# Performance work log

Hardware: AMD Instinct MI355X
Metric: run time of the kernel (lower is better)

## Reference

```python
import jax, jax.numpy as jnp
import numpy as np

N = 100000   # nodes
E = 1600000  # directed edges (avg degree 16)
H = 64       # MODEL_HIDDEN_CHANNELS


def setup_inputs() -> dict:
    key = jax.random.key(0)
    ks = jax.random.split(key, 6)
    x = jax.random.normal(ks[0], (N, 1), dtype=jnp.float32)
    edge_index = jax.random.randint(ks[1], (2, E), 0, N, dtype=jnp.int32)
    w1 = jax.random.normal(ks[2], (1, H), dtype=jnp.float32) * 0.5
    b1 = jnp.zeros((H,), dtype=jnp.float32)
    w2 = jax.random.normal(ks[3], (H, H), dtype=jnp.float32) * (1.0 / np.sqrt(H))
    b2 = jnp.zeros((H,), dtype=jnp.float32)
    wfc = jax.random.normal(ks[4], (H, 1), dtype=jnp.float32) * (1.0 / np.sqrt(H))
    bfc = jnp.zeros((1,), dtype=jnp.float32)
    return {"x": x, "edge_index": edge_index, "w1": w1, "b1": b1,
            "w2": w2, "b2": b2, "wfc": wfc, "bfc": bfc}


def _gcn_conv(x, src, dst, norm, W, b, n):
    # PyG GCNConv: h = x @ W, then scatter-add of norm-weighted messages at dst, + bias
    h = x @ W                                   # [n, out]
    msg = h[src] * norm[:, None]                # gather + scale, [e, out]
    agg = jax.ops.segment_sum(msg, dst, num_segments=n)
    return agg + b


def reference(x, edge_index, w1, b1, w2, b2, wfc, bfc):
    n = x.shape[0]
    # add self-loops (PyG GCNConv default)
    loops = jnp.arange(n, dtype=edge_index.dtype)
    src = jnp.concatenate([edge_index[0], loops])
    dst = jnp.concatenate([edge_index[1], loops])
    # symmetric degree normalization D^{-1/2} A_hat D^{-1/2}
    deg = jax.ops.segment_sum(jnp.ones(src.shape[0], dtype=x.dtype), dst, num_segments=n)
    dinv = jnp.where(deg > 0, jax.lax.rsqrt(deg), 0.0)
    norm = dinv[src] * dinv[dst]
    h = jax.nn.relu(_gcn_conv(x, src, dst, norm, w1, b1, n))
    h = jax.nn.relu(_gcn_conv(h, src, dst, norm, w2, b2, n))
    out = h @ wfc + bfc                         # [n, 1]
    return out.reshape(-1)
```

## Files before the change

kernel.cpp:

```cpp
#include <hip/hip_runtime.h>


#define HCH 64
#define CHUNK 8192
#define BSH 7
#define BSZ 128
#define NBMAX 1024

__device__ __forceinline__ void lds_addf(float* p, float v) {
    __hip_atomic_fetch_add(p, v, __ATOMIC_RELAXED, __HIP_MEMORY_SCOPE_WORKGROUP);
}

__global__ __launch_bounds__(512) void k_init(int nb, int cap,
                                              int* __restrict__ cursor,
                                              int* __restrict__ ov_cursor,
                                              const float* __restrict__ w1,
                                              const float* __restrict__ b1,
                                              const float* __restrict__ w2,
                                              float* __restrict__ P) {
    __shared__ float part[8][4][HCH];
    __shared__ float fsum;
    int t = threadIdx.x;
    for (int i = t; i < nb; i += 512) cursor[i] = i * cap;
    if (t == 0) { *ov_cursor = 0; fsum = 0.f; }
    int j = t & 63, seg = t >> 6;
    float pp = 0.f, pm = 0.f, bp = 0.f, bm = 0.f;
#pragma unroll
    for (int kk = 0; kk < 8; kk++) {
        int k = seg * 8 + kk;
        float w = w1[k], b = b1[k], v = w2[k * HCH + j];
        if (w > 0.f) { pp += w * v; bp += b * v; }
        else if (w < 0.f) { pm += w * v; bm += b * v; }
        else { float rb = b > 0.f ? b : 0.f; bp += rb * v; bm += rb * v; }
    }
    part[seg][0][j] = pp; part[seg][1][j] = pm;
    part[seg][2][j] = bp; part[seg][3][j] = bm;
    __syncthreads();
    if (t < 4 * HCH) {
        int c = t >> 6, jj = t & 63;
        float s = 0.f;
#pragma unroll
        for (int g = 0; g < 8; g++) s += part[g][c][jj];
        P[t] = s;
        if (c >= 2) lds_addf(&fsum, fabsf(s));
    }
    __syncthreads();
    if (t == 0) P[4 * HCH] = fsum;
}

__global__ __launch_bounds__(512) void k_place(const int* __restrict__ src,
                                               const int* __restrict__ dst, int e,
                                               int nb, int cap,
                                               int* __restrict__ cursor,
                                               int* __restrict__ ov_cursor,
                                               int* __restrict__ packed,
                                               int2* __restrict__ ovbuf) {
    __shared__ int h[NBMAX];
    __shared__ int scanE[NBMAX];
    __shared__ int basel[NBMAX];
    __shared__ int avail[NBMAX];
    __shared__ int slpv[CHUNK];
    __shared__ short ssb[CHUNK];
    __shared__ int wsum[8];
    int t = threadIdx.x;
    for (int i = t; i < NBMAX; i += 512) h[i] = 0;
    __syncthreads();
    int cbase = blockIdx.x * CHUNK;
    int rem = min(e - cbase, CHUNK);

#pragma unroll
    for (int k = 0; k < CHUNK / 2048; k++) {
        int li = (k * 512 + t) * 4;
        if (li + 3 < rem) {
            int4 d4 = *(const int4*)(dst + cbase + li);
            atomicAdd(&h[d4.x >> BSH], 1);
            atomicAdd(&h[d4.y >> BSH], 1);
            atomicAdd(&h[d4.z >> BSH], 1);
            atomicAdd(&h[d4.w >> BSH], 1);
        } else {
            for (int q = li; q < rem && q < li + 4; q++)
                atomicAdd(&h[dst[cbase + q] >> BSH], 1);
        }
    }
    __syncthreads();

    int v0 = h[2 * t], v1 = h[2 * t + 1];
    for (int i = t; i < nb; i += 512) {
        int my = h[i];
        int av = 0, base = 0;
        if (my) {
            base = atomicAdd(&cursor[i], my);
            int room = (i + 1) * cap - base;
            av = room < 0 ? 0 : (room > my ? my : room);
        }
        basel[i] = base;
        avail[i] = av;
    }
    int lane = t & 63, wid = t >> 6;
    int s = v0 + v1;
    int incl = s;
#pragma unroll
    for (int d = 1; d < 64; d <<= 1) {
        int o = __shfl_up(incl, d, 64);
        if (lane >= d) incl += o;
    }
    if (lane == 63) wsum[wid] = incl;
    __syncthreads();
    if (t < 8) {
        int v = wsum[t];
        int inc2 = v;
#pragma unroll
        for (int d = 1; d < 8; d <<= 1) {
            int o = __shfl_up(inc2, d, 8);
            if (t >= d) inc2 += o;
        }
        wsum[t] = inc2 - v;
    }
    for (int i = t; i < NBMAX; i += 512) h[i] = 0;
    __syncthreads();
    int excl = incl - s + wsum[wid];
    scanE[2 * t] = excl;
    scanE[2 * t + 1] = excl + v0;
    __syncthreads();

#pragma unroll
    for (int k = 0; k < CHUNK / 2048; k++) {
        int li = (k * 512 + t) * 4;
        if (li + 3 < rem) {
            int4 s4 = *(const int4*)(src + cbase + li);
            int4 d4 = *(const int4*)(dst + cbase + li);
#pragma unroll
            for (int q = 0; q < 4; q++) {
                int sv = (q == 0) ? s4.x : (q == 1) ? s4.y : (q == 2) ? s4.z : s4.w;
                int dv = (q == 0) ? d4.x : (q == 1) ? d4.y : (q == 2) ? d4.z : d4.w;
                int b = dv >> BSH;
                int pos = scanE[b] + atomicAdd(&h[b], 1);
                slpv[pos] = sv | ((dv & (BSZ - 1)) << 17);
                ssb[pos] = (short)b;
            }
        } else {
            for (int q = li; q < rem && q < li + 4; q++) {
                int sv = src[cbase + q], dv = dst[cbase + q];
                int b = dv >> BSH;
                int pos = scanE[b] + atomicAdd(&h[b], 1);
                slpv[pos] = sv | ((dv & (BSZ - 1)) << 17);
                ssb[pos] = (short)b;
            }
        }
    }
    __syncthreads();

    for (int jj = t; jj < rem; jj += 512) {
        int b = ssb[jj];
        int loc = jj - scanE[b];
        int pv = slpv[jj];
        if (loc < avail[b]) {
            packed[basel[b] + loc] = pv;
        } else {
            int op = atomicAdd(ov_cursor, 1);
            ovbuf[op] = make_int2(pv & 0x1FFFF, (b << BSH) | (pv >> 17));
        }
    }
}

__global__ __launch_bounds__(512) void k_bdeg(const int* __restrict__ packed,
                                              const int* __restrict__ cursor,
                                              const int* __restrict__ ov_cursor,
                                              const int2* __restrict__ ovbuf,
                                              int cap, const float* __restrict__ x, int n,
                                              float* __restrict__ dinv,
                                              float* __restrict__ y) {
    __shared__ int cnt[BSZ];
    int bk = blockIdx.x, t = threadIdx.x;
    int bbase = bk * cap;
    int bcnt = min(cursor[bk] - bbase, cap);
    if (t < BSZ) cnt[t] = 0;
    __syncthreads();
    for (int base = 0; base < bcnt; base += 2048) {
        int i0 = base + t * 4;
        if (i0 + 3 < bcnt) {
            int4 p = *(const int4*)(packed + bbase + i0);
            atomicAdd(&cnt[p.x >> 17], 1);
            atomicAdd(&cnt[p.y >> 17], 1);
            atomicAdd(&cnt[p.z >> 17], 1);
            atomicAdd(&cnt[p.w >> 17], 1);
        } else {
            for (int i = i0; i < bcnt && i < i0 + 4; i++)
                atomicAdd(&cnt[packed[bbase + i] >> 17], 1);
        }
    }
    int ovc = *ov_cursor;
    for (int i = t; i < ovc; i += 512) {
        int2 o = ovbuf[i];
        if ((o.y >> BSH) == bk) atomicAdd(&cnt[o.y & (BSZ - 1)], 1);
    }
    __syncthreads();
    int node = (bk << BSH) + t;
    if (t < BSZ && node < n) {
        float dv = rsqrtf((float)(cnt[t] + 1));
        dinv[node] = dv;
        y[node] = dv * x[node];
    }
}

__global__ __launch_bounds__(512) void k_bagg1(const int* __restrict__ packed,
                                               const int* __restrict__ cursor,
                                               const int* __restrict__ ov_cursor,
                                               const int2* __restrict__ ovbuf,
                                               int cap,
                                               const float* __restrict__ dinv,
                                               const float* __restrict__ y, int n,
                                               float2* __restrict__ val2) {
    __shared__ float acc[BSZ];
    int bk = blockIdx.x, t = threadIdx.x;
    int bbase = bk * cap;
    int bcnt = min(cursor[bk] - bbase, cap);
    if (t < BSZ) acc[t] = 0.f;
    __syncthreads();
    for (int base = 0; base < bcnt; base += 2048) {
        int i0 = base + t * 4;
        if (i0 + 3 < bcnt) {
            int4 p = *(const int4*)(packed + bbase + i0);
            float y0 = y[p.x & 0x1FFFF], y1 = y[p.y & 0x1FFFF];
            float y2 = y[p.z & 0x1FFFF], y3 = y[p.w & 0x1FFFF];
            lds_addf(&acc[p.x >> 17], y0);
            lds_addf(&acc[p.y >> 17], y1);
            lds_addf(&acc[p.z >> 17], y2);
            lds_addf(&acc[p.w >> 17], y3);
        } else {
            for (int i = i0; i < bcnt && i < i0 + 4; i++) {
                int p = packed[bbase + i];
                lds_addf(&acc[p >> 17], y[p & 0x1FFFF]);
            }
        }
    }
    int ovc = *ov_cursor;
    for (int i = t; i < ovc; i += 512) {
        int2 o = ovbuf[i];
        if ((o.y >> BSH) == bk) lds_addf(&acc[o.y & (BSZ - 1)], y[o.x]);
    }
    __syncthreads();
    int node = (bk << BSH) + t;
    if (t < BSZ && node < n) {
        float dv = dinv[node];
        float s = dv * (acc[t] + y[node]);
        val2[node] = make_float2(dv * s, dv);
    }
}

__global__ __launch_bounds__(512) void k_bagg2(const int* __restrict__ packed,
                                               const int* __restrict__ cursor,
                                               const int* __restrict__ ov_cursor,
                                               const int2* __restrict__ ovbuf,
                                               int cap, const float2* __restrict__ val2,
                                               const float* __restrict__ dinv,
                                               const float* __restrict__ P,
                                               const float* __restrict__ b2,
                                               const float* __restrict__ wfc,
                                               const float* __restrict__ bfc,
                                               float* __restrict__ out, int n) {
    __shared__ float aa[2 * BSZ];
    __shared__ float cc[2 * BSZ];
    __shared__ float sP[4 * HCH], sb2[HCH], swfc[HCH];
    __shared__ float sflag;
    int bk = blockIdx.x, t = threadIdx.x;
    int bbase = bk * cap;
    int bcnt = min(cursor[bk] - bbase, cap);
    if (t < 2 * BSZ) { aa[t] = 0.f; cc[t] = 0.f; }
    if (t < 4 * HCH) sP[t] = P[t];
    if (t >= 256 && t < 320) sb2[t - 256] = b2[t - 256];
    if (t >= 320 && t < 384) swfc[t - 320] = wfc[t - 320];
    if (t == 448) sflag = P[4 * HCH];
    __syncthreads();
    bool useB = sflag != 0.f;
    for (int base = 0; base < bcnt; base += 2048) {
        int i0 = base + t * 4;
        if (i0 + 3 < bcnt) {
            int4 p = *(const int4*)(packed + bbase + i0);
            float2 v0 = val2[p.x & 0x1FFFF], v1 = val2[p.y & 0x1FFFF];
            float2 v2 = val2[p.z & 0x1FFFF], v3 = val2[p.w & 0x1FFFF];
            int o0 = (v0.x > 0.f ? 0 : BSZ) + (p.x >> 17);
            int o1 = (v1.x > 0.f ? 0 : BSZ) + (p.y >> 17);
            int o2 = (v2.x > 0.f ? 0 : BSZ) + (p.z >> 17);
            int o3 = (v3.x > 0.f ? 0 : BSZ) + (p.w >> 17);
            lds_addf(&aa[o0], v0.x); lds_addf(&aa[o1], v1.x);
            lds_addf(&aa[o2], v2.x); lds_addf(&aa[o3], v3.x);
            if (useB) {
                lds_addf(&cc[o0], v0.y); lds_addf(&cc[o1], v1.y);
                lds_addf(&cc[o2], v2.y); lds_addf(&cc[o3], v3.y);
            }
        } else {
            for (int i = i0; i < bcnt && i < i0 + 4; i++) {
                int p = packed[bbase + i];
                float2 v = val2[p & 0x1FFFF];
                int off = (v.x > 0.f ? 0 : BSZ) + (p >> 17);
                lds_addf(&aa[off], v.x);
                if (useB) lds_addf(&cc[off], v.y);
            }
        }
    }
    int ovc = *ov_cursor;
    for (int i = t; i < ovc; i += 512) {
        int2 o = ovbuf[i];
        if ((o.y >> BSH) == bk) {
            float2 v = val2[o.x];
            int off = (v.x > 0.f ? 0 : BSZ) + (o.y & (BSZ - 1));
            lds_addf(&aa[off], v.x);
            if (useB) lds_addf(&cc[off], v.y);
        }
    }
    __syncthreads();
    int node = (bk << BSH) + t;
    if (t >= BSZ || node >= n) return;
    float a_p = aa[t], a_m = aa[BSZ + t], c_p = cc[t], c_m = cc[BSZ + t];
    float2 sv = val2[node];
    if (sv.x > 0.f) { a_p += sv.x; c_p += sv.y; }
    else            { a_m += sv.x; c_m += sv.y; }
    float dv = dinv[node];
    float acc = 0.f;
#pragma unroll 8
    for (int j = 0; j < HCH; j++) {
        float z = dv * (a_p * sP[j] + a_m * sP[HCH + j] +
                        c_p * sP[2 * HCH + j] + c_m * sP[3 * HCH + j]) + sb2[j];
        z = z > 0.f ? z : 0.f;
        acc += z * swfc[j];
    }
    out[node] = acc + bfc[0];
}

extern "C" void kernel_launch(void* const* d_in, const int* in_sizes, int n_in,
                              void* d_out, int out_size, void* d_ws, size_t ws_size,
                              hipStream_t stream) {
    const float* x   = (const float*)d_in[0];
    const int*   ei  = (const int*)d_in[1];
    const float* w1  = (const float*)d_in[2];
    const float* b1  = (const float*)d_in[3];
    const float* w2  = (const float*)d_in[4];
    const float* b2  = (const float*)d_in[5];
    const float* wfc = (const float*)d_in[6];
    const float* bfc = (const float*)d_in[7];
    float* out = (float*)d_out;

    const int n = in_sizes[0];
    const int e = in_sizes[1] / 2;
    const int* src = ei;
    const int* dst = ei + e;

    const int nb = (n + BSZ - 1) >> BSH;
    int avg = (e + nb - 1) / nb;
    int cap = ((avg + avg / 4 + 64) + 15) & ~15;

    auto al = [](size_t v) { return (v + 255) & ~(size_t)255; };
    char* ws = (char*)d_ws;
    size_t o = 0;
    int* cursor    = (int*)(ws + o);  o = al(o + (size_t)NBMAX * 4);
    int* ov_cursor = (int*)(ws + o);  o = al(o + 256);
    float* dinv  = (float*)(ws + o);  o = al(o + (size_t)n * 4);
    float* y     = (float*)(ws + o);  o = al(o + (size_t)n * 4);
    float2* val2 = (float2*)(ws + o); o = al(o + (size_t)n * 8);
    float* P     = (float*)(ws + o);  o = al(o + (4 * HCH + 8) * 4);
    int* packed  = (int*)(ws + o);    o = al(o + (size_t)nb * cap * 4);
    int2* ovbuf  = (int2*)(ws + o);   o = al(o + (size_t)e * 8);
    (void)ws_size;

    const int nchunk = (e + CHUNK - 1) / CHUNK;

    k_init<<<1, 512, 0, stream>>>(nb, cap, cursor, ov_cursor, w1, b1, w2, P);
    k_place<<<nchunk, 512, 0, stream>>>(src, dst, e, nb, cap, cursor, ov_cursor,
                                        packed, ovbuf);
    k_bdeg<<<nb, 512, 0, stream>>>(packed, cursor, ov_cursor, ovbuf, cap, x, n, dinv, y);
    k_bagg1<<<nb, 512, 0, stream>>>(packed, cursor, ov_cursor, ovbuf, cap, dinv, y,
                                    n, val2);
    k_bagg2<<<nb, 512, 0, stream>>>(packed, cursor, ov_cursor, ovbuf, cap, val2, dinv,
                                    P, b2, wfc, bfc, out, n);
}
```

Before: 129.5 us.

## Drop init kernel, fold weight precompute into bagg2, halve place chunk

Removes the single-block init kernel. Cursor and overflow-counter reset now uses a memset with block-relative cursors, and every k_bagg2 block recomputes the folded W1·W2 projection table in shared memory. k_place uses chunks half as large, with each thread handling 8 edges in one pass and src/dst loaded once up front and reused for both the histogram and scatter phases. The bagg2 epilogue splits the 64-channel dot product across 4 threads per node, with a shared-memory reduction. The aim is to cut a serial tiny launch and raise parallelism, at the cost of redundant per-block weight math and more place blocks doing global cursor atomics.

```diff
diff --git a/kernel.cpp b/kernel.cpp
--- a/kernel.cpp
+++ b/kernel.cpp
@@ -2,7 +2,7 @@
 
 
 #define HCH 64
-#define CHUNK 8192
+#define CHUNK 4096
 #define BSH 7
 #define BSZ 128
 #define NBMAX 1024
@@ -11,47 +11,10 @@
     __hip_atomic_fetch_add(p, v, __ATOMIC_RELAXED, __HIP_MEMORY_SCOPE_WORKGROUP);
 }
 
-__global__ __launch_bounds__(512) void k_init(int nb, int cap,
-                                              int* __restrict__ cursor,
-                                              int* __restrict__ ov_cursor,
-                                              const float* __restrict__ w1,
-                                              const float* __restrict__ b1,
-                                              const float* __restrict__ w2,
-                                              float* __restrict__ P) {
-    __shared__ float part[8][4][HCH];
-    __shared__ float fsum;
-    int t = threadIdx.x;
-    for (int i = t; i < nb; i += 512) cursor[i] = i * cap;
-    if (t == 0) { *ov_cursor = 0; fsum = 0.f; }
-    int j = t & 63, seg = t >> 6;
-    float pp = 0.f, pm = 0.f, bp = 0.f, bm = 0.f;
-#pragma unroll
-    for (int kk = 0; kk < 8; kk++) {
-        int k = seg * 8 + kk;
-        float w = w1[k], b = b1[k], v = w2[k * HCH + j];
-        if (w > 0.f) { pp += w * v; bp += b * v; }
-        else if (w < 0.f) { pm += w * v; bm += b * v; }
-        else { float rb = b > 0.f ? b : 0.f; bp += rb * v; bm += rb * v; }
-    }
-    part[seg][0][j] = pp; part[seg][1][j] = pm;
-    part[seg][2][j] = bp; part[seg][3][j] = bm;
-    __syncthreads();
-    if (t < 4 * HCH) {
-        int c = t >> 6, jj = t & 63;
-        float s = 0.f;
-#pragma unroll
-        for (int g = 0; g < 8; g++) s += part[g][c][jj];
-        P[t] = s;
-        if (c >= 2) lds_addf(&fsum, fabsf(s));
-    }
-    __syncthreads();
-    if (t == 0) P[4 * HCH] = fsum;
-}
-
 __global__ __launch_bounds__(512) void k_place(const int* __restrict__ src,
                                                const int* __restrict__ dst, int e,
                                                int nb, int cap,
-                                               int* __restrict__ cursor,
+                                               int* __restrict__ cursorRel,
                                                int* __restrict__ ov_cursor,
                                                int* __restrict__ packed,
                                                int2* __restrict__ ovbuf) {
@@ -67,20 +30,22 @@
     __syncthreads();
     int cbase = blockIdx.x * CHUNK;
     int rem = min(e - cbase, CHUNK);
-
-#pragma unroll
-    for (int k = 0; k < CHUNK / 2048; k++) {
-        int li = (k * 512 + t) * 4;
-        if (li + 3 < rem) {
-            int4 d4 = *(const int4*)(dst + cbase + li);
-            atomicAdd(&h[d4.x >> BSH], 1);
-            atomicAdd(&h[d4.y >> BSH], 1);
-            atomicAdd(&h[d4.z >> BSH], 1);
-            atomicAdd(&h[d4.w >> BSH], 1);
-        } else {
-            for (int q = li; q < rem && q < li + 4; q++)
-                atomicAdd(&h[dst[cbase + q] >> BSH], 1);
-        }
+    int li = t * 8;
+    bool fast = (li + 7 < rem);
+
+    int4 sA, sB, dA, dB;
+    if (fast) {
+        sA = *(const int4*)(src + cbase + li);
+        sB = *(const int4*)(src + cbase + li + 4);
+        dA = *(const int4*)(dst + cbase + li);
+        dB = *(const int4*)(dst + cbase + li + 4);
+        atomicAdd(&h[dA.x >> BSH], 1); atomicAdd(&h[dA.y >> BSH], 1);
+        atomicAdd(&h[dA.z >> BSH], 1); atomicAdd(&h[dA.w >> BSH], 1);
+        atomicAdd(&h[dB.x >> BSH], 1); atomicAdd(&h[dB.y >> BSH], 1);
+        atomicAdd(&h[dB.z >> BSH], 1); atomicAdd(&h[dB.w >> BSH], 1);
+    } else {
+        for (int q = li; q < rem && q < li + 8; q++)
+            atomicAdd(&h[dst[cbase + q] >> BSH], 1);
     }
     __syncthreads();
 
@@ -89,8 +54,9 @@
         int my = h[i];
         int av = 0, base = 0;
         if (my) {
-            base = atomicAdd(&cursor[i], my);
-            int room = (i + 1) * cap - base;
+            int baseRel = atomicAdd(&cursorRel[i], my);
+            base = i * cap + baseRel;
+            int room = cap - baseRel;
             av = room < 0 ? 0 : (room > my ? my : room);
         }
         basel[i] = base;
@@ -123,29 +89,27 @@
     scanE[2 * t + 1] = excl + v0;
     __syncthreads();
 
-#pragma unroll
-    for (int k = 0; k < CHUNK / 2048; k++) {
-        int li = (k * 512 + t) * 4;
-        if (li + 3 < rem) {
-            int4 s4 = *(const int4*)(src + cbase + li);
-            int4 d4 = *(const int4*)(dst + cbase + li);
-#pragma unroll
-            for (int q = 0; q < 4; q++) {
-                int sv = (q == 0) ? s4.x : (q == 1) ? s4.y : (q == 2) ? s4.z : s4.w;
-                int dv = (q == 0) ? d4.x : (q == 1) ? d4.y : (q == 2) ? d4.z : d4.w;
-                int b = dv >> BSH;
-                int pos = scanE[b] + atomicAdd(&h[b], 1);
-                slpv[pos] = sv | ((dv & (BSZ - 1)) << 17);
-                ssb[pos] = (short)b;
-            }
-        } else {
-            for (int q = li; q < rem && q < li + 4; q++) {
-                int sv = src[cbase + q], dv = dst[cbase + q];
-                int b = dv >> BSH;
-                int pos = scanE[b] + atomicAdd(&h[b], 1);
-                slpv[pos] = sv | ((dv & (BSZ - 1)) << 17);
-                ssb[pos] = (short)b;
-            }
+    if (fast) {
+#pragma unroll
+        for (int q = 0; q < 8; q++) {
+            int sv = (q == 0) ? sA.x : (q == 1) ? sA.y : (q == 2) ? sA.z :
+                     (q == 3) ? sA.w : (q == 4) ? sB.x : (q == 5) ? sB.y :
+                     (q == 6) ? sB.z : sB.w;
+            int dv = (q == 0) ? dA.x : (q == 1) ? dA.y : (q == 2) ? dA.z :
+                     (q == 3) ? dA.w : (q == 4) ? dB.x : (q == 5) ? dB.y :
+                     (q == 6) ? dB.z : dB.w;
+            int b = dv >> BSH;
+            int pos = scanE[b] + atomicAdd(&h[b], 1);
+            slpv[pos] = sv | ((dv & (BSZ - 1)) << 17);
+            ssb[pos] = (short)b;
+        }
+    } else {
+        for (int q = li; q < rem && q < li + 8; q++) {
+            int sv = src[cbase + q], dv = dst[cbase + q];
+            int b = dv >> BSH;
+            int pos = scanE[b] + atomicAdd(&h[b], 1);
+            slpv[pos] = sv | ((dv & (BSZ - 1)) << 17);
+            ssb[pos] = (short)b;
         }
     }
     __syncthreads();
@@ -164,7 +128,7 @@
 }
 
 __global__ __launch_bounds__(512) void k_bdeg(const int* __restrict__ packed,
-                                              const int* __restrict__ cursor,
+                                              const int* __restrict__ cursorRel,
                                               const int* __restrict__ ov_cursor,
                                               const int2* __restrict__ ovbuf,
                                               int cap, const float* __restrict__ x, int n,
@@ -173,7 +137,7 @@
     __shared__ int cnt[BSZ];
     int bk = blockIdx.x, t = threadIdx.x;
     int bbase = bk * cap;
-    int bcnt = min(cursor[bk] - bbase, cap);
+    int bcnt = min(cursorRel[bk], cap);
     if (t < BSZ) cnt[t] = 0;
     __syncthreads();
     for (int base = 0; base < bcnt; base += 2048) {
@@ -204,7 +168,7 @@
 }
 
 __global__ __launch_bounds__(512) void k_bagg1(const int* __restrict__ packed,
-                                               const int* __restrict__ cursor,
+                                               const int* __restrict__ cursorRel,
                                                const int* __restrict__ ov_cursor,
                                                const int2* __restrict__ ovbuf,
                                                int cap,
@@ -214,7 +178,7 @@
     __shared__ float acc[BSZ];
     int bk = blockIdx.x, t = threadIdx.x;
     int bbase = bk * cap;
-    int bcnt = min(cursor[bk] - bbase, cap);
+    int bcnt = min(cursorRel[bk], cap);
     if (t < BSZ) acc[t] = 0.f;
     __syncthreads();
     for (int base = 0; base < bcnt; base += 2048) {
@@ -249,30 +213,58 @@
 }
 
 __global__ __launch_bounds__(512) void k_bagg2(const int* __restrict__ packed,
-                                               const int* __restrict__ cursor,
+                                               const int* __restrict__ cursorRel,
                                                const int* __restrict__ ov_cursor,
                                                const int2* __restrict__ ovbuf,
                                                int cap, const float2* __restrict__ val2,
                                                const float* __restrict__ dinv,
-                                               const float* __restrict__ P,
+                                               const float* __restrict__ w1,
+                                               const float* __restrict__ b1,
+                                               const float* __restrict__ w2,
                                                const float* __restrict__ b2,
                                                const float* __restrict__ wfc,
                                                const float* __restrict__ bfc,
                                                float* __restrict__ out, int n) {
     __shared__ float aa[2 * BSZ];
     __shared__ float cc[2 * BSZ];
+    __shared__ float part[8][4][HCH];
     __shared__ float sP[4 * HCH], sb2[HCH], swfc[HCH];
-    __shared__ float sflag;
+    __shared__ float part2[4][BSZ];
+    __shared__ float fsum;
     int bk = blockIdx.x, t = threadIdx.x;
     int bbase = bk * cap;
-    int bcnt = min(cursor[bk] - bbase, cap);
-    if (t < 2 * BSZ) { aa[t] = 0.f; cc[t] = 0.f; }
-    if (t < 4 * HCH) sP[t] = P[t];
+    int bcnt = min(cursorRel[bk], cap);
+
+    {
+        int j = t & 63, seg = t >> 6;
+        float pp = 0.f, pm = 0.f, bp = 0.f, bm = 0.f;
+#pragma unroll
+        for (int kk = 0; kk < 8; kk++) {
+            int k = seg * 8 + kk;
+            float w = w1[k], b = b1[k], v = w2[k * HCH + j];
+            if (w > 0.f) { pp += w * v; bp += b * v; }
+            else if (w < 0.f) { pm += w * v; bm += b * v; }
+            else { float rb = b > 0.f ? b : 0.f; bp += rb * v; bm += rb * v; }
+        }
+        part[seg][0][j] = pp; part[seg][1][j] = pm;
+        part[seg][2][j] = bp; part[seg][3][j] = bm;
+    }
+    if (t < 256) aa[t] = 0.f; else cc[t - 256] = 0.f;
     if (t >= 256 && t < 320) sb2[t - 256] = b2[t - 256];
     if (t >= 320 && t < 384) swfc[t - 320] = wfc[t - 320];
-    if (t == 448) sflag = P[4 * HCH];
-    __syncthreads();
-    bool useB = sflag != 0.f;
+    if (t == 448) fsum = 0.f;
+    __syncthreads();
+    if (t < 4 * HCH) {
+        int c = t >> 6, jj = t & 63;
+        float ssum = 0.f;
+#pragma unroll
+        for (int g = 0; g < 8; g++) ssum += part[g][c][jj];
+        sP[t] = ssum;
+        if (c >= 2) lds_addf(&fsum, fabsf(ssum));
+    }
+    __syncthreads();
+    bool useB = fsum != 0.f;
+
     for (int base = 0; base < bcnt; base += 2048) {
         int i0 = base + t * 4;
         if (i0 + 3 < bcnt) {
@@ -310,22 +302,33 @@
         }
     }
     __syncthreads();
-    int node = (bk << BSH) + t;
-    if (t >= BSZ || node >= n) return;
-    float a_p = aa[t], a_m = aa[BSZ + t], c_p = cc[t], c_m = cc[BSZ + t];
-    float2 sv = val2[node];
-    if (sv.x > 0.f) { a_p += sv.x; c_p += sv.y; }
-    else            { a_m += sv.x; c_m += sv.y; }
-    float dv = dinv[node];
-    float acc = 0.f;
-#pragma unroll 8
-    for (int j = 0; j < HCH; j++) {
-        float z = dv * (a_p * sP[j] + a_m * sP[HCH + j] +
-                        c_p * sP[2 * HCH + j] + c_m * sP[3 * HCH + j]) + sb2[j];
-        z = z > 0.f ? z : 0.f;
-        acc += z * swfc[j];
-    }
-    out[node] = acc + bfc[0];
+
+    int tt = t & (BSZ - 1), q = t >> 7;
+    int node = (bk << BSH) + tt;
+    if (node < n) {
+        float a_p = aa[tt], a_m = aa[BSZ + tt];
+        float c_p = cc[tt], c_m = cc[BSZ + tt];
+        float2 sv = val2[node];
+        if (sv.x > 0.f) { a_p += sv.x; c_p += sv.y; }
+        else            { a_m += sv.x; c_m += sv.y; }
+        float dv = dinv[node];
+        float pacc = 0.f;
+#pragma unroll
+        for (int u = 0; u < 16; u++) {
+            int j = q * 16 + u;
+            float z = dv * (a_p * sP[j] + a_m * sP[HCH + j] +
+                            c_p * sP[2 * HCH + j] + c_m * sP[3 * HCH + j]) + sb2[j];
+            z = z > 0.f ? z : 0.f;
+            pacc += z * swfc[j];
+        }
+        part2[q][tt] = pacc;
+    }
+    __syncthreads();
+    if (t < BSZ) {
+        int nd = (bk << BSH) + t;
+        if (nd < n)
+            out[nd] = part2[0][t] + part2[1][t] + part2[2][t] + part2[3][t] + bfc[0];
+    }
 }
 
 extern "C" void kernel_launch(void* const* d_in, const int* in_sizes, int n_in,
@@ -353,24 +356,24 @@
     auto al = [](size_t v) { return (v + 255) & ~(size_t)255; };
     char* ws = (char*)d_ws;
     size_t o = 0;
-    int* cursor    = (int*)(ws + o);  o = al(o + (size_t)NBMAX * 4);
+    int* cursorRel = (int*)(ws + o);  o = al(o + (size_t)NBMAX * 4);
     int* ov_cursor = (int*)(ws + o);  o = al(o + 256);
     float* dinv  = (float*)(ws + o);  o = al(o + (size_t)n * 4);
     float* y     = (float*)(ws + o);  o = al(o + (size_t)n * 4);
     float2* val2 = (float2*)(ws + o); o = al(o + (size_t)n * 8);
-    float* P     = (float*)(ws + o);  o = al(o + (4 * HCH + 8) * 4);
     int* packed  = (int*)(ws + o);    o = al(o + (size_t)nb * cap * 4);
     int2* ovbuf  = (int2*)(ws + o);   o = al(o + (size_t)e * 8);
     (void)ws_size;
 
     const int nchunk = (e + CHUNK - 1) / CHUNK;
 
-    k_init<<<1, 512, 0, stream>>>(nb, cap, cursor, ov_cursor, w1, b1, w2, P);
-    k_place<<<nchunk, 512, 0, stream>>>(src, dst, e, nb, cap, cursor, ov_cursor,
+    hipMemsetAsync(ws, 0, (size_t)NBMAX * 4 + 4, stream);
+    k_place<<<nchunk, 512, 0, stream>>>(src, dst, e, nb, cap, cursorRel, ov_cursor,
                                         packed, ovbuf);
-    k_bdeg<<<nb, 512, 0, stream>>>(packed, cursor, ov_cursor, ovbuf, cap, x, n, dinv, y);
-    k_bagg1<<<nb, 512, 0, stream>>>(packed, cursor, ov_cursor, ovbuf, cap, dinv, y,
+    k_bdeg<<<nb, 512, 0, stream>>>(packed, cursorRel, ov_cursor, ovbuf, cap, x, n,
+                                   dinv, y);
+    k_bagg1<<<nb, 512, 0, stream>>>(packed, cursorRel, ov_cursor, ovbuf, cap, dinv, y,
                                     n, val2);
-    k_bagg2<<<nb, 512, 0, stream>>>(packed, cursor, ov_cursor, ovbuf, cap, val2, dinv,
-                                    P, b2, wfc, bfc, out, n);
-}
+    k_bagg2<<<nb, 512, 0, stream>>>(packed, cursorRel, ov_cursor, ovbuf, cap, val2,
+                                    dinv, w1, b1, w2, b2, wfc, bfc, out, n);
+}
```

After: 134.3 us. +3.7%, slower.
